# Kernel optimization log

Hardware: AMD Instinct MI355X
Metric: run time of the kernel (lower is better)

## Reference

```python
import jax, jax.numpy as jnp
import numpy as np

N_EMBD = 768
N_HEAD = 12
DIM_HEAD = N_EMBD // N_HEAD


def setup_inputs() -> dict:
    key = jax.random.key(0)
    k1, k2, k3 = jax.random.split(key, 3)
    B, T = 4, 2048
    x = jax.random.normal(k1, (B, T, N_EMBD), dtype=jnp.float32)
    # torch Linear(n_embd, 3*n_embd, bias=False): y = x @ W.T, W:[3C,C].
    # Store pre-transposed [C,3C] for direct matmul.
    s = 1.0 / np.sqrt(N_EMBD)
    W_qkv = jax.random.uniform(k2, (N_EMBD, 3 * N_EMBD), dtype=jnp.float32, minval=-s, maxval=s)
    W_proj = jax.random.uniform(k3, (N_EMBD, N_EMBD), dtype=jnp.float32, minval=-s, maxval=s)
    return {"x": x, "W_qkv": W_qkv, "W_proj": W_proj}


def reference(x, W_qkv, W_proj):
    B, T, C = x.shape
    qkv = x @ W_qkv                                  # [B,T,3C]
    q, k, v = jnp.split(qkv, 3, axis=-1)
    def heads(t):  # [B,T,C] -> [B,H,T,Dh]
        return t.reshape(B, T, N_HEAD, DIM_HEAD).transpose(0, 2, 1, 3)
    q, k, v = heads(q), heads(k), heads(v)
    # Source divides by scale = dim_head**-0.5, i.e. multiplies by sqrt(dim_head).
    scores = jnp.einsum('bhtd,bhsd->bhts', q, k) * jnp.sqrt(jnp.float32(DIM_HEAD))
    attn = jax.nn.softmax(scores, axis=-1)           # [B,H,T,T] materialized
    y = jnp.einsum('bhts,bhsd->bhtd', attn, v)       # [B,H,T,Dh]
    y = y.transpose(0, 2, 1, 3).reshape(B, T, C)
    return y @ W_proj
```

## Files before the change

kernel.cpp:

```cpp
#include <hip/hip_runtime.h>

typedef _Float16 f16;
typedef f16 f16x4 __attribute__((ext_vector_type(4)));
typedef f16 f16x8 __attribute__((ext_vector_type(8)));
typedef __fp16 h16x2 __attribute__((ext_vector_type(2)));
typedef float floatx4 __attribute__((ext_vector_type(4)));

#define LDT 72
#define LDE 136
#define QSCALE 11.5415603271117f

__device__ __forceinline__ void gld16(const void* g, void* l) {
  __builtin_amdgcn_global_load_lds((const __attribute__((address_space(1))) unsigned int*)g,
                                   (__attribute__((address_space(3))) unsigned int*)l,
                                   16, 0, 0);
}

__global__ __launch_bounds__(256) void cvt_f32_f16(const float* __restrict__ in,
                                                   f16* __restrict__ out) {
  size_t i = ((size_t)blockIdx.x * 256 + threadIdx.x) * 8;
  float4 v0 = *(const float4*)(in + i);
  float4 v1 = *(const float4*)(in + i + 4);
  f16x8 h = {(f16)v0.x, (f16)v0.y, (f16)v0.z, (f16)v0.w,
             (f16)v1.x, (f16)v1.y, (f16)v1.z, (f16)v1.w};
  *(f16x8*)(out + i) = h;
}

__global__ __launch_bounds__(256) void transpose_f32_f16_tiled(const float* __restrict__ in,
                                                               f16* __restrict__ out,
                                                               int K, int N) {
  __shared__ f16 tile[64][LDT];
  int k0 = blockIdx.x * 64, n0 = blockIdx.y * 64;
  int tid = threadIdx.x;
  int r = tid >> 4, c4 = (tid & 15) * 4;
  for (int p = 0; p < 4; ++p) {
    int rr = r + p * 16;
    float4 v = *(const float4*)(in + (size_t)(k0 + rr) * N + n0 + c4);
    tile[c4 + 0][rr] = (f16)v.x;
    tile[c4 + 1][rr] = (f16)v.y;
    tile[c4 + 2][rr] = (f16)v.z;
    tile[c4 + 3][rr] = (f16)v.w;
  }
  __syncthreads();
  int rn = tid >> 3, ck = (tid & 7) * 8;
  for (int p = 0; p < 2; ++p) {
    int rr = rn + p * 32;
    *(uint4*)(out + (size_t)(n0 + rr) * K + k0 + ck) = *(const uint4*)(&tile[rr][ck]);
  }
}

__global__ __launch_bounds__(256) void gemm1_qkv(const f16* __restrict__ A,
                                                 const f16* __restrict__ Bt,
                                                 f16* __restrict__ q16, f16* __restrict__ k16,
                                                 f16* __restrict__ vt) {
  __shared__ f16 smem[17408];
  f16* As = smem;
  f16* Bs = smem + 8192;
  int tid = threadIdx.x;
  int lane = tid & 63, wid = tid >> 6;
  int quad = lane >> 4, l16 = lane & 15;
  int wy = wid >> 1, wx = wid & 1;
  int m0 = blockIdx.x * 128, n0 = blockIdx.y * 128;
  int gr = lane >> 3, gc = (lane & 7) * 8;
  floatx4 acc[4][4] = {};
  for (int k0 = 0; k0 < 768; k0 += 64) {
    for (int p = 0; p < 4; ++p) {
      int c = wid * 4 + p;
      int row = c * 8 + gr;
      gld16(A + (size_t)(m0 + row) * 768 + k0 + gc, As + c * 512);
      gld16(Bt + (size_t)(n0 + row) * 768 + k0 + gc, Bs + c * 512);
    }
    __syncthreads();
    for (int kk = 0; kk < 64; kk += 32) {
      f16x8 af[4], bfr[4];
      for (int i = 0; i < 4; ++i)
        af[i] = *(const f16x8*)(As + (wy * 64 + i * 16 + l16) * 64 + kk + quad * 8);
      for (int j = 0; j < 4; ++j)
        bfr[j] = *(const f16x8*)(Bs + (wx * 64 + j * 16 + l16) * 64 + kk + quad * 8);
      for (int i = 0; i < 4; ++i)
        for (int j = 0; j < 4; ++j)
          acc[i][j] = __builtin_amdgcn_mfma_f32_16x16x32_f16(af[i], bfr[j], acc[i][j], 0, 0, 0);
    }
    __syncthreads();
  }
  int b = m0 >> 11, t0 = m0 & 2047;
  if (n0 < 1536) {
    for (int i = 0; i < 4; ++i)
      for (int j = 0; j < 4; ++j)
        for (int r = 0; r < 4; ++r) {
          int t = t0 + wy * 64 + i * 16 + quad * 4 + r;
          int col = n0 + wx * 64 + j * 16 + l16;
          float a = acc[i][j][r];
          if (col < 768) {
            int h = col >> 6, d = col & 63;
            q16[((size_t)(b * 12 + h)) * 131072 + (size_t)t * 64 + d] = (f16)(a * QSCALE);
          } else {
            int c = col - 768;
            int h = c >> 6, d = c & 63;
            k16[((size_t)(b * 12 + h)) * 131072 + (size_t)t * 64 + d] = (f16)a;
          }
        }
  } else {
    f16* Vtile = smem;
    int h0 = (n0 - 1536) >> 6;
    for (int i = 0; i < 4; ++i)
      for (int j = 0; j < 4; ++j) {
        int cl = wx * 64 + j * 16 + l16;
        int rl = wy * 64 + i * 16 + quad * 4;
        for (int r = 0; r < 4; ++r)
          Vtile[cl * LDE + rl + r] = (f16)acc[i][j][r];
      }
    __syncthreads();
    int u = tid & 15;
    for (int p = 0; p < 8; ++p) {
      int c = (tid >> 4) + p * 16;
      *(uint4*)(vt + ((size_t)(b * 12 + h0 + (c >> 6))) * 131072 +
                (size_t)(c & 63) * 2048 + t0 + u * 8) =
          *(const uint4*)(Vtile + c * LDE + u * 8);
    }
  }
}

__global__ __launch_bounds__(256) void gemm_bt_f16(const f16* __restrict__ A,
                                                   const f16* __restrict__ Bt,
                                                   float* __restrict__ C,
                                                   int M, int N, int K) {
  __shared__ f16 As[8192];
  __shared__ f16 Bs[8192];
  int tid = threadIdx.x;
  int lane = tid & 63, wid = tid >> 6;
  int quad = lane >> 4, l16 = lane & 15;
  int wy = wid >> 1, wx = wid & 1;
  int m0 = blockIdx.x * 128, n0 = blockIdx.y * 128;
  int gr = lane >> 3, gc = (lane & 7) * 8;
  floatx4 acc[4][4] = {};
  for (int k0 = 0; k0 < K; k0 += 64) {
    for (int p = 0; p < 4; ++p) {
      int c = wid * 4 + p;
      int row = c * 8 + gr;
      gld16(A + (size_t)(m0 + row) * K + k0 + gc, As + c * 512);
      gld16(Bt + (size_t)(n0 + row) * K + k0 + gc, Bs + c * 512);
    }
    __syncthreads();
    for (int kk = 0; kk < 64; kk += 32) {
      f16x8 af[4], bfr[4];
      for (int i = 0; i < 4; ++i)
        af[i] = *(const f16x8*)(As + (wy * 64 + i * 16 + l16) * 64 + kk + quad * 8);
      for (int j = 0; j < 4; ++j)
        bfr[j] = *(const f16x8*)(Bs + (wx * 64 + j * 16 + l16) * 64 + kk + quad * 8);
      for (int i = 0; i < 4; ++i)
        for (int j = 0; j < 4; ++j)
          acc[i][j] = __builtin_amdgcn_mfma_f32_16x16x32_f16(af[i], bfr[j], acc[i][j], 0, 0, 0);
    }
    __syncthreads();
  }
  for (int i = 0; i < 4; ++i) {
    int row = m0 + wy * 64 + i * 16 + quad * 4;
    for (int j = 0; j < 4; ++j) {
      int col = n0 + wx * 64 + j * 16 + l16;
      for (int r = 0; r < 4; ++r)
        C[(size_t)(row + r) * N + col] = acc[i][j][r];
    }
  }
}

__global__ __launch_bounds__(512, 1) void flash_attn(const f16* __restrict__ q16,
                                                     const f16* __restrict__ k16,
                                                     const f16* __restrict__ vT,
                                                     f16* __restrict__ y) {
  __shared__ f16 Ks[128 * 64];
  __shared__ f16 Vt[64 * 128];
  const int T = 2048;
  int xcd = blockIdx.x & 7, yb = blockIdx.x >> 3;
  int bh = xcd * 6 + (yb >> 4);
  int qt = yb & 15;
  int b = bh / 12, h = bh - b * 12;
  int tid = threadIdx.x;
  int lane = tid & 63, wid = tid >> 6;
  int quad = lane >> 4, l16 = lane & 15;
  int rk = tid >> 3, kch = tid & 7;
  int rv = tid >> 4, vch = tid & 15;
  int kswz = (kch ^ (rk & 7)) * 8;
  int vswz = (vch ^ (rv & 15)) * 8;
  size_t hb = (size_t)bh * T * 64;

  f16x8 qf[2];
  {
    size_t qrow = hb + (size_t)(qt * 128 + wid * 16 + l16) * 64 + quad * 8;
    qf[0] = *(const f16x8*)(q16 + qrow);
    qf[1] = *(const f16x8*)(q16 + qrow + 32);
  }
  f16x4 ones4;
  for (int e = 0; e < 4; ++e) ones4[e] = (f16)1.0f;

  float m_i = -1e30f, l_i = 0.f;
  floatx4 o[4] = {};

  for (int kt = 0; kt < 16; ++kt) {
    if (kt) __syncthreads();
    for (int p = 0; p < 2; ++p) {
      int r = rk + p * 64;
      *(uint4*)(Ks + r * 64 + kswz) =
          *(const uint4*)(k16 + hb + (size_t)(kt * 128 + r) * 64 + kch * 8);
      int d = rv + p * 32;
      *(uint4*)(Vt + d * 128 + vswz) =
          *(const uint4*)(vT + hb + (size_t)d * T + kt * 128 + vch * 8);
    }
    __syncthreads();

    floatx4 sf[8];
    const floatx4 z4 = {0.f, 0.f, 0.f, 0.f};
    for (int i = 0; i < 8; ++i) sf[i] = z4;
    for (int kk = 0; kk < 2; ++kk)
      for (int i = 0; i < 8; ++i) {
        int row = i * 16 + l16;
        f16x8 kf = *(const f16x8*)(Ks + row * 64 + (((kk * 4 + quad) ^ (l16 & 7)) * 8));
        sf[i] = __builtin_amdgcn_mfma_f32_16x16x32_f16(kf, qf[kk], sf[i], 0, 0, 0);
      }

    float mx = fmaxf(fmaxf(sf[0][0], sf[0][1]), fmaxf(sf[0][2], sf[0][3]));
    for (int i = 1; i < 8; ++i)
      mx = fmaxf(mx, fmaxf(fmaxf(sf[i][0], sf[i][1]), fmaxf(sf[i][2], sf[i][3])));
    mx = fmaxf(mx, __shfl_xor(mx, 16));
    mx = fmaxf(mx, __shfl_xor(mx, 32));
    float m_new = fmaxf(m_i, mx);
    float alpha = exp2f(m_i - m_new);
    m_i = m_new;
    for (int i = 0; i < 4; ++i) o[i] *= alpha;

    f16x4 pf[8];
    for (int i = 0; i < 8; ++i) {
      union { h16x2 h; f16 f[2]; } a2, b2;
      a2.h = __builtin_amdgcn_cvt_pkrtz(sf[i][0] - m_new, sf[i][1] - m_new);
      b2.h = __builtin_amdgcn_cvt_pkrtz(sf[i][2] - m_new, sf[i][3] - m_new);
      f16x4 uu = {a2.f[0], a2.f[1], b2.f[0], b2.f[1]};
#if __has_builtin(__builtin_elementwise_exp2)
      pf[i] = __builtin_elementwise_exp2(uu);
#else
      for (int r = 0; r < 4; ++r) pf[i][r] = (f16)exp2f((float)uu[r]);
#endif
    }

    floatx4 rs = z4;
    for (int si = 0; si < 8; ++si)
      rs = __builtin_amdgcn_mfma_f32_16x16x16f16(ones4, pf[si], rs, 0, 0, 0);
    l_i = l_i * alpha + rs[0];

    for (int i = 0; i < 4; ++i)
      for (int si = 0; si < 8; ++si) {
        int d = i * 16 + l16;
        int cch = si * 2 + (quad >> 1);
        f16x4 vf = *(const f16x4*)(Vt + d * 128 + ((cch ^ l16) * 8) + (quad & 1) * 4);
        o[i] = __builtin_amdgcn_mfma_f32_16x16x16f16(vf, pf[si], o[i], 0, 0, 0);
      }
  }

  float invl = 1.0f / l_i;
  int t = qt * 128 + wid * 16 + l16;
  size_t off = ((size_t)(b * T + t)) * 768 + h * 64;
  for (int i = 0; i < 4; ++i)
    for (int r = 0; r < 4; ++r)
      y[off + i * 16 + quad * 4 + r] = (f16)(o[i][r] * invl);
}

extern "C" void kernel_launch(void* const* d_in, const int* in_sizes, int n_in,
                              void* d_out, int out_size, void* d_ws, size_t ws_size,
                              hipStream_t stream) {
  const float* x     = (const float*)d_in[0];
  const float* Wqkv  = (const float*)d_in[1];
  const float* Wproj = (const float*)d_in[2];
  float* out = (float*)d_out;
  char* ws = (char*)d_ws;
  f16* q16    = (f16*)ws;
  f16* k16    = (f16*)(ws + 12582912);
  f16* vT16   = (f16*)(ws + 25165824);
  f16* y16    = (f16*)(ws + 37748736);
  f16* WqkvT  = (f16*)(ws + 50331648);
  f16* WprojT = (f16*)(ws + 53870592);
  f16* x16 = y16;

  cvt_f32_f16<<<3072, 256, 0, stream>>>(x, x16);
  transpose_f32_f16_tiled<<<dim3(12, 36), 256, 0, stream>>>(Wqkv, WqkvT, 768, 2304);
  transpose_f32_f16_tiled<<<dim3(12, 12), 256, 0, stream>>>(Wproj, WprojT, 768, 768);
  gemm1_qkv<<<dim3(64, 18), 256, 0, stream>>>(x16, WqkvT, q16, k16, vT16);
  flash_attn<<<768, 512, 0, stream>>>(q16, k16, vT16, y16);
  gemm_bt_f16<<<dim3(64, 6), 256, 0, stream>>>(y16, WprojT, out, 8192, 768, 768);
}
```

Measured before the change: 250.8 us.

## Double-buffer K/V tiles with async global-to-LDS loads in flash attention

The flash attention kernel moves from 512 threads with 16 query rows per wave to 256 threads with 32 query rows per wave, so each K/V fragment read from LDS feeds two query groups. K and V tiles are now double-buffered in LDS and filled with direct global-to-LDS loads, so the next tile streams in while the current one is computed. This targets load latency and LDS read traffic, at the cost of twice the LDS footprint, more registers per wave, and fewer waves per block.

```diff
diff --git a/kernel.cpp b/kernel.cpp
--- a/kernel.cpp
+++ b/kernel.cpp
@@ -164,12 +164,14 @@
   }
 }
 
-__global__ __launch_bounds__(512, 1) void flash_attn(const f16* __restrict__ q16,
+__global__ __launch_bounds__(256, 1) void flash_attn(const f16* __restrict__ q16,
                                                      const f16* __restrict__ k16,
                                                      const f16* __restrict__ vT,
                                                      f16* __restrict__ y) {
-  __shared__ f16 Ks[128 * 64];
-  __shared__ f16 Vt[64 * 128];
+  __shared__ f16 KsA[128 * 64];
+  __shared__ f16 VtA[64 * 128];
+  __shared__ f16 KsB[128 * 64];
+  __shared__ f16 VtB[64 * 128];
   const int T = 2048;
   int xcd = blockIdx.x & 7, yb = blockIdx.x >> 3;
   int bh = xcd * 6 + (yb >> 4);
@@ -178,89 +180,117 @@
   int tid = threadIdx.x;
   int lane = tid & 63, wid = tid >> 6;
   int quad = lane >> 4, l16 = lane & 15;
-  int rk = tid >> 3, kch = tid & 7;
-  int rv = tid >> 4, vch = tid & 15;
-  int kswz = (kch ^ (rk & 7)) * 8;
-  int vswz = (vch ^ (rv & 15)) * 8;
   size_t hb = (size_t)bh * T * 64;
 
-  f16x8 qf[2];
+  int kr = lane >> 3;
+  int kcc = ((lane & 7) ^ kr) * 8;
+  const f16* kbase = k16 + hb + (size_t)(wid * 32 + kr) * 64 + kcc;
+  const f16* vbase0;
+  const f16* vbase1;
+  const f16* vbase2;
+  const f16* vbase3;
   {
-    size_t qrow = hb + (size_t)(qt * 128 + wid * 16 + l16) * 64 + quad * 8;
-    qf[0] = *(const f16x8*)(q16 + qrow);
-    qf[1] = *(const f16x8*)(q16 + qrow + 32);
+    int lr = lane >> 4, lc = lane & 15;
+    vbase0 = vT + hb + (size_t)(wid * 16 + 0 + lr) * T + ((lc ^ (0 + lr)) * 8);
+    vbase1 = vT + hb + (size_t)(wid * 16 + 4 + lr) * T + ((lc ^ (4 + lr)) * 8);
+    vbase2 = vT + hb + (size_t)(wid * 16 + 8 + lr) * T + ((lc ^ (8 + lr)) * 8);
+    vbase3 = vT + hb + (size_t)(wid * 16 + 12 + lr) * T + ((lc ^ (12 + lr)) * 8);
+  }
+
+#define STAGE(KD, VD, ktn)                                              \
+  do {                                                                  \
+    const f16* kp_ = kbase + (size_t)(ktn) * 8192;                      \
+    gld16(kp_ + 0 * 512, (KD) + (wid * 4 + 0) * 512);                   \
+    gld16(kp_ + 1 * 512, (KD) + (wid * 4 + 1) * 512);                   \
+    gld16(kp_ + 2 * 512, (KD) + (wid * 4 + 2) * 512);                   \
+    gld16(kp_ + 3 * 512, (KD) + (wid * 4 + 3) * 512);                   \
+    gld16(vbase0 + (ktn) * 128, (VD) + (wid * 4 + 0) * 512);            \
+    gld16(vbase1 + (ktn) * 128, (VD) + (wid * 4 + 1) * 512);            \
+    gld16(vbase2 + (ktn) * 128, (VD) + (wid * 4 + 2) * 512);            \
+    gld16(vbase3 + (ktn) * 128, (VD) + (wid * 4 + 3) * 512);            \
+  } while (0)
+
+  f16x8 qf[2][2];
+#pragma unroll
+  for (int g = 0; g < 2; ++g) {
+    size_t qrow = hb + (size_t)(qt * 128 + wid * 32 + g * 16 + l16) * 64 + quad * 8;
+    qf[g][0] = *(const f16x8*)(q16 + qrow);
+    qf[g][1] = *(const f16x8*)(q16 + qrow + 32);
   }
   f16x4 ones4;
   for (int e = 0; e < 4; ++e) ones4[e] = (f16)1.0f;
 
-  float m_i = -1e30f, l_i = 0.f;
-  floatx4 o[4] = {};
-
-  for (int kt = 0; kt < 16; ++kt) {
-    if (kt) __syncthreads();
-    for (int p = 0; p < 2; ++p) {
-      int r = rk + p * 64;
-      *(uint4*)(Ks + r * 64 + kswz) =
-          *(const uint4*)(k16 + hb + (size_t)(kt * 128 + r) * 64 + kch * 8);
-      int d = rv + p * 32;
-      *(uint4*)(Vt + d * 128 + vswz) =
-          *(const uint4*)(vT + hb + (size_t)d * T + kt * 128 + vch * 8);
-    }
-    __syncthreads();
-
-    floatx4 sf[8];
-    const floatx4 z4 = {0.f, 0.f, 0.f, 0.f};
-    for (int i = 0; i < 8; ++i) sf[i] = z4;
-    for (int kk = 0; kk < 2; ++kk)
-      for (int i = 0; i < 8; ++i) {
-        int row = i * 16 + l16;
-        f16x8 kf = *(const f16x8*)(Ks + row * 64 + (((kk * 4 + quad) ^ (l16 & 7)) * 8));
-        sf[i] = __builtin_amdgcn_mfma_f32_16x16x32_f16(kf, qf[kk], sf[i], 0, 0, 0);
-      }
-
-    float mx = fmaxf(fmaxf(sf[0][0], sf[0][1]), fmaxf(sf[0][2], sf[0][3]));
-    for (int i = 1; i < 8; ++i)
-      mx = fmaxf(mx, fmaxf(fmaxf(sf[i][0], sf[i][1]), fmaxf(sf[i][2], sf[i][3])));
-    mx = fmaxf(mx, __shfl_xor(mx, 16));
-    mx = fmaxf(mx, __shfl_xor(mx, 32));
-    float m_new = fmaxf(m_i, mx);
-    float alpha = exp2f(m_i - m_new);
-    m_i = m_new;
-    for (int i = 0; i < 4; ++i) o[i] *= alpha;
-
-    f16x4 pf[8];
-    for (int i = 0; i < 8; ++i) {
-      union { h16x2 h; f16 f[2]; } a2, b2;
-      a2.h = __builtin_amdgcn_cvt_pkrtz(sf[i][0] - m_new, sf[i][1] - m_new);
-      b2.h = __builtin_amdgcn_cvt_pkrtz(sf[i][2] - m_new, sf[i][3] - m_new);
-      f16x4 uu = {a2.f[0], a2.f[1], b2.f[0], b2.f[1]};
-#if __has_builtin(__builtin_elementwise_exp2)
-      pf[i] = __builtin_elementwise_exp2(uu);
-#else
-      for (int r = 0; r < 4; ++r) pf[i][r] = (f16)exp2f((float)uu[r]);
-#endif
-    }
-
-    floatx4 rs = z4;
-    for (int si = 0; si < 8; ++si)
-      rs = __builtin_amdgcn_mfma_f32_16x16x16f16(ones4, pf[si], rs, 0, 0, 0);
-    l_i = l_i * alpha + rs[0];
-
+  float m_i[2] = {-1e30f, -1e30f}, l_i[2] = {0.f, 0.f};
+  floatx4 o[2][4] = {};
+
+#define COMPUTE(KC, VC)                                                            \
+  do {                                                                             \
+    floatx4 sf[2][8] = {};                                                         \
+    _Pragma("unroll") for (int kk = 0; kk < 2; ++kk)                               \
+        _Pragma("unroll") for (int i = 0; i < 8; ++i) {                            \
+      f16x8 kf = *(const f16x8*)((KC) + (i * 16 + l16) * 64 +                      \
+                                 (((kk * 4 + quad) ^ (l16 & 7)) * 8));             \
+      sf[0][i] = __builtin_amdgcn_mfma_f32_16x16x32_f16(kf, qf[0][kk], sf[0][i], 0, 0, 0); \
+      sf[1][i] = __builtin_amdgcn_mfma_f32_16x16x32_f16(kf, qf[1][kk], sf[1][i], 0, 0, 0); \
+    }                                                                              \
+    f16x4 pf[2][8];                                                                \
+    _Pragma("unroll") for (int g = 0; g < 2; ++g) {                                \
+      float mx = fmaxf(fmaxf(sf[g][0][0], sf[g][0][1]), fmaxf(sf[g][0][2], sf[g][0][3])); \
+      _Pragma("unroll") for (int i = 1; i < 8; ++i)                                \
+          mx = fmaxf(mx, fmaxf(fmaxf(sf[g][i][0], sf[g][i][1]),                    \
+                               fmaxf(sf[g][i][2], sf[g][i][3])));                  \
+      mx = fmaxf(mx, __shfl_xor(mx, 16));                                          \
+      mx = fmaxf(mx, __shfl_xor(mx, 32));                                          \
+      float m_new = fmaxf(m_i[g], mx);                                             \
+      float alpha = exp2f(m_i[g] - m_new);                                         \
+      m_i[g] = m_new;                                                              \
+      _Pragma("unroll") for (int i = 0; i < 4; ++i) o[g][i] *= alpha;              \
+      _Pragma("unroll") for (int i = 0; i < 8; ++i) {                              \
+        union { h16x2 hh; f16 ff[2]; } a2, b2;                                     \
+        a2.hh = __builtin_amdgcn_cvt_pkrtz(sf[g][i][0] - m_new, sf[g][i][1] - m_new); \
+        b2.hh = __builtin_amdgcn_cvt_pkrtz(sf[g][i][2] - m_new, sf[g][i][3] - m_new); \
+        f16x4 uu = {a2.ff[0], a2.ff[1], b2.ff[0], b2.ff[1]};                       \
+        pf[g][i] = __builtin_elementwise_exp2(uu);                                 \
+      }                                                                            \
+      floatx4 rs = {0.f, 0.f, 0.f, 0.f};                                           \
+      _Pragma("unroll") for (int si = 0; si < 8; ++si)                             \
+          rs = __builtin_amdgcn_mfma_f32_16x16x16f16(ones4, pf[g][si], rs, 0, 0, 0); \
+      l_i[g] = l_i[g] * alpha + rs[0];                                             \
+    }                                                                              \
+    _Pragma("unroll") for (int i = 0; i < 4; ++i)                                  \
+        _Pragma("unroll") for (int si = 0; si < 8; ++si) {                         \
+      int cch = si * 2 + (quad >> 1);                                              \
+      f16x4 vf = *(const f16x4*)((VC) + (i * 16 + l16) * 128 + ((cch ^ l16) * 8) + \
+                                 (quad & 1) * 4);                                  \
+      o[0][i] = __builtin_amdgcn_mfma_f32_16x16x16f16(vf, pf[0][si], o[0][i], 0, 0, 0); \
+      o[1][i] = __builtin_amdgcn_mfma_f32_16x16x16f16(vf, pf[1][si], o[1][i], 0, 0, 0); \
+    }                                                                              \
+  } while (0)
+
+  STAGE(KsA, VtA, 0);
+  __syncthreads();
+
+#pragma unroll 1
+  for (int kt2 = 0; kt2 < 8; ++kt2) {
+    STAGE(KsB, VtB, 2 * kt2 + 1);
+    COMPUTE(KsA, VtA);
+    __syncthreads();
+    if (kt2 < 7) STAGE(KsA, VtA, 2 * kt2 + 2);
+    COMPUTE(KsB, VtB);
+    if (kt2 < 7) __syncthreads();
+  }
+
+#pragma unroll
+  for (int g = 0; g < 2; ++g) {
+    float invl = 1.0f / l_i[g];
+    int t = qt * 128 + wid * 32 + g * 16 + l16;
+    size_t off = ((size_t)(b * T + t)) * 768 + h * 64;
     for (int i = 0; i < 4; ++i)
-      for (int si = 0; si < 8; ++si) {
-        int d = i * 16 + l16;
-        int cch = si * 2 + (quad >> 1);
-        f16x4 vf = *(const f16x4*)(Vt + d * 128 + ((cch ^ l16) * 8) + (quad & 1) * 4);
-        o[i] = __builtin_amdgcn_mfma_f32_16x16x16f16(vf, pf[si], o[i], 0, 0, 0);
-      }
-  }
-
-  float invl = 1.0f / l_i;
-  int t = qt * 128 + wid * 16 + l16;
-  size_t off = ((size_t)(b * T + t)) * 768 + h * 64;
-  for (int i = 0; i < 4; ++i)
-    for (int r = 0; r < 4; ++r)
-      y[off + i * 16 + quad * 4 + r] = (f16)(o[i][r] * invl);
+      for (int r = 0; r < 4; ++r)
+        y[off + i * 16 + quad * 4 + r] = (f16)(o[g][i][r] * invl);
+  }
+#undef STAGE
+#undef COMPUTE
 }
 
 extern "C" void kernel_launch(void* const* d_in, const int* in_sizes, int n_in,
@@ -283,6 +313,6 @@
   transpose_f32_f16_tiled<<<dim3(12, 36), 256, 0, stream>>>(Wqkv, WqkvT, 768, 2304);
   transpose_f32_f16_tiled<<<dim3(12, 12), 256, 0, stream>>>(Wproj, WprojT, 768, 768);
   gemm1_qkv<<<dim3(64, 18), 256, 0, stream>>>(x16, WqkvT, q16, k16, vT16);
-  flash_attn<<<768, 512, 0, stream>>>(q16, k16, vT16, y16);
+  flash_attn<<<768, 256, 0, stream>>>(q16, k16, vT16, y16);
   gemm_bt_f16<<<dim3(64, 6), 256, 0, stream>>>(y16, WprojT, out, 8192, 768, 768);
 }
```

Result: no change. 253.4 us (+1.0%).

## Double-buffer GEMM LDS tiles and XOR-swizzle them to avoid bank conflicts

Applied to the files above, without the earlier changes.

Both f16 GEMM kernels (the QKV projection and the output projection) now use two LDS buffers. The global-to-LDS loads for the next 64-wide K slice are issued before computing on the current one, so memory latency overlaps with MFMA work and there is one barrier per slice. The LDS layout is XOR-swizzled by row, both in the load source column and in the fragment read address, to cut bank conflicts on the 16-byte fragment reads. LDS use per block doubles to 64KB, which can lower occupancy.

```diff
diff --git a/kernel.cpp b/kernel.cpp
--- a/kernel.cpp
+++ b/kernel.cpp
@@ -49,40 +49,63 @@
   }
 }
 
+
+#define GEMM_DEFS                                                        \
+  int tid = threadIdx.x;                                                 \
+  int lane = tid & 63, wid = tid >> 6;                                   \
+  int quad = lane >> 4, l16 = lane & 15;                                 \
+  int wy = wid >> 1, wx = wid & 1;                                       \
+  int m0 = blockIdx.x * 128, n0 = blockIdx.y * 128;                      \
+  int gr = lane >> 3;                                                    \
+  int gcs = ((lane & 7) ^ gr) * 8;
+
+#define STG(AOFF, BOFF, K0)                                              \
+  do {                                                                   \
+    _Pragma("unroll") for (int p = 0; p < 4; ++p) {                      \
+      gld16(aSrc + (size_t)p * 8 * strA + (K0), smem + (AOFF) + (wid * 4 + p) * 512); \
+      gld16(bSrc + (size_t)p * 8 * strB + (K0), smem + (BOFF) + (wid * 4 + p) * 512); \
+    }                                                                    \
+  } while (0)
+
+#define CMP(AOFF, BOFF)                                                  \
+  do {                                                                   \
+    _Pragma("unroll") for (int kk8 = 0; kk8 < 8; kk8 += 4) {             \
+      f16x8 af[4], bfr[4];                                               \
+      _Pragma("unroll") for (int i = 0; i < 4; ++i)                      \
+        af[i] = *(const f16x8*)(smem + (AOFF) + (wy * 64 + i * 16 + l16) * 64 + \
+                                (((kk8 + quad) ^ (l16 & 7)) * 8));       \
+      _Pragma("unroll") for (int j = 0; j < 4; ++j)                      \
+        bfr[j] = *(const f16x8*)(smem + (BOFF) + (wx * 64 + j * 16 + l16) * 64 + \
+                                 (((kk8 + quad) ^ (l16 & 7)) * 8));      \
+      _Pragma("unroll") for (int i = 0; i < 4; ++i)                      \
+        _Pragma("unroll") for (int j = 0; j < 4; ++j)                    \
+          acc[i][j] = __builtin_amdgcn_mfma_f32_16x16x32_f16(af[i], bfr[j], acc[i][j], 0, 0, 0); \
+    }                                                                    \
+  } while (0)
+
 __global__ __launch_bounds__(256) void gemm1_qkv(const f16* __restrict__ A,
                                                  const f16* __restrict__ Bt,
                                                  f16* __restrict__ q16, f16* __restrict__ k16,
                                                  f16* __restrict__ vt) {
-  __shared__ f16 smem[17408];
-  f16* As = smem;
-  f16* Bs = smem + 8192;
-  int tid = threadIdx.x;
-  int lane = tid & 63, wid = tid >> 6;
-  int quad = lane >> 4, l16 = lane & 15;
-  int wy = wid >> 1, wx = wid & 1;
-  int m0 = blockIdx.x * 128, n0 = blockIdx.y * 128;
-  int gr = lane >> 3, gc = (lane & 7) * 8;
+  __shared__ f16 smem[32768];
+  GEMM_DEFS
+  const int strA = 768, strB = 768;
+  const f16* aSrc = A + (size_t)(m0 + wid * 32 + gr) * 768 + gcs;
+  const f16* bSrc = Bt + (size_t)(n0 + wid * 32 + gr) * 768 + gcs;
   floatx4 acc[4][4] = {};
-  for (int k0 = 0; k0 < 768; k0 += 64) {
-    for (int p = 0; p < 4; ++p) {
-      int c = wid * 4 + p;
-      int row = c * 8 + gr;
-      gld16(A + (size_t)(m0 + row) * 768 + k0 + gc, As + c * 512);
-      gld16(Bt + (size_t)(n0 + row) * 768 + k0 + gc, Bs + c * 512);
-    }
-    __syncthreads();
-    for (int kk = 0; kk < 64; kk += 32) {
-      f16x8 af[4], bfr[4];
-      for (int i = 0; i < 4; ++i)
-        af[i] = *(const f16x8*)(As + (wy * 64 + i * 16 + l16) * 64 + kk + quad * 8);
-      for (int j = 0; j < 4; ++j)
-        bfr[j] = *(const f16x8*)(Bs + (wx * 64 + j * 16 + l16) * 64 + kk + quad * 8);
-      for (int i = 0; i < 4; ++i)
-        for (int j = 0; j < 4; ++j)
-          acc[i][j] = __builtin_amdgcn_mfma_f32_16x16x32_f16(af[i], bfr[j], acc[i][j], 0, 0, 0);
-    }
-    __syncthreads();
-  }
+
+  STG(0, 8192, 0);
+  __syncthreads();
+#pragma unroll 1
+  for (int k2 = 0; k2 < 6; ++k2) {
+    STG(16384, 24576, (2 * k2 + 1) * 64);
+    CMP(0, 8192);
+    __syncthreads();
+    if (k2 < 5) STG(0, 8192, (2 * k2 + 2) * 64);
+    CMP(16384, 24576);
+    __syncthreads();
+  }
+
   int b = m0 >> 11, t0 = m0 & 2047;
   if (n0 < 1536) {
     for (int i = 0; i < 4; ++i)
@@ -125,35 +148,26 @@
                                                    const f16* __restrict__ Bt,
                                                    float* __restrict__ C,
                                                    int M, int N, int K) {
-  __shared__ f16 As[8192];
-  __shared__ f16 Bs[8192];
-  int tid = threadIdx.x;
-  int lane = tid & 63, wid = tid >> 6;
-  int quad = lane >> 4, l16 = lane & 15;
-  int wy = wid >> 1, wx = wid & 1;
-  int m0 = blockIdx.x * 128, n0 = blockIdx.y * 128;
-  int gr = lane >> 3, gc = (lane & 7) * 8;
+  __shared__ f16 smem[32768];
+  GEMM_DEFS
+  const int strA = K, strB = K;
+  const f16* aSrc = A + (size_t)(m0 + wid * 32 + gr) * K + gcs;
+  const f16* bSrc = Bt + (size_t)(n0 + wid * 32 + gr) * K + gcs;
   floatx4 acc[4][4] = {};
-  for (int k0 = 0; k0 < K; k0 += 64) {
-    for (int p = 0; p < 4; ++p) {
-      int c = wid * 4 + p;
-      int row = c * 8 + gr;
-      gld16(A + (size_t)(m0 + row) * K + k0 + gc, As + c * 512);
-      gld16(Bt + (size_t)(n0 + row) * K + k0 + gc, Bs + c * 512);
-    }
-    __syncthreads();
-    for (int kk = 0; kk < 64; kk += 32) {
-      f16x8 af[4], bfr[4];
-      for (int i = 0; i < 4; ++i)
-        af[i] = *(const f16x8*)(As + (wy * 64 + i * 16 + l16) * 64 + kk + quad * 8);
-      for (int j = 0; j < 4; ++j)
-        bfr[j] = *(const f16x8*)(Bs + (wx * 64 + j * 16 + l16) * 64 + kk + quad * 8);
-      for (int i = 0; i < 4; ++i)
-        for (int j = 0; j < 4; ++j)
-          acc[i][j] = __builtin_amdgcn_mfma_f32_16x16x32_f16(af[i], bfr[j], acc[i][j], 0, 0, 0);
-    }
-    __syncthreads();
-  }
+  int nk2 = K >> 7;
+
+  STG(0, 8192, 0);
+  __syncthreads();
+#pragma unroll 1
+  for (int k2 = 0; k2 < nk2; ++k2) {
+    STG(16384, 24576, (2 * k2 + 1) * 64);
+    CMP(0, 8192);
+    __syncthreads();
+    if (k2 < nk2 - 1) STG(0, 8192, (2 * k2 + 2) * 64);
+    CMP(16384, 24576);
+    __syncthreads();
+  }
+
   for (int i = 0; i < 4; ++i) {
     int row = m0 + wy * 64 + i * 16 + quad * 4;
     for (int j = 0; j < 4; ++j) {
```

Measured after the change: 228.0 us. 1.1x faster.
